# Kernel optimization log

Hardware: AMD Instinct MI355X
Metric: run time of the kernel (lower is better)

The kernel has to match this reference:

```python
import jax, jax.numpy as jnp
import numpy as np

NEG_FILL = -1000000.0


def setup_inputs() -> dict:
    key = jax.random.key(0)
    k1, k2, k3, k4, k5 = jax.random.split(key, 5)
    bs, sl, hd, dd = 128, 512, 1024, 512
    x = jax.random.normal(k1, (bs, sl, hd), dtype=jnp.float32)
    mask = jax.random.randint(k2, (bs, sl), 0, 2) > 0  # bool, True = masked out
    Wq = jax.random.normal(k3, (dd, hd), dtype=jnp.float32)
    bq = jax.random.normal(k4, (dd,), dtype=jnp.float32)
    vq = jax.random.normal(k5, (dd,), dtype=jnp.float32)
    return {"x": x, "mask": mask, "Wq": Wq, "bq": bq, "vq": vq}


def reference(x, mask, Wq, bq, vq):
    # key = tanh(Uq(x)): [bs, sl, dd]
    k = jnp.tanh(jnp.einsum("bsh,dh->bsd", x, Wq) + bq)
    # score = vq . key: [bs, sl]
    score = jnp.einsum("bsd,d->bs", k, vq)
    score = jnp.where(mask, NEG_FILL, score)
    weight = jax.nn.softmax(score, axis=-1)  # [bs, sl]
    # weighted sum over sequence: [bs, hd]
    res = jnp.einsum("bs,bsh->bh", weight, x)
    return res
```

## Files before the change

### kernel.cpp

```cpp
#include <hip/hip_runtime.h>
#include <stdint.h>

#define BS 128
#define SL 512
#define HD 1024
#define DD 512
#define M_TOT (BS*SL)

typedef __attribute__((ext_vector_type(8))) short short8;
typedef __attribute__((ext_vector_type(4))) float f32x4;

__device__ __forceinline__ unsigned short f32_bf16(float f) {
    union { float f; unsigned u; } v; v.f = f;
    unsigned u = v.u + 0x7FFFu + ((v.u >> 16) & 1u);
    return (unsigned short)(u >> 16);
}
__device__ __forceinline__ float bf16_f32(unsigned short h) {
    union { unsigned u; float f; } v; v.u = ((unsigned)h) << 16; return v.f;
}

__global__ void detect_mask_kernel(const unsigned* mw, int* flag) {
    int t = threadIdx.x;
    unsigned bad = 0;
    for (int i = t; i < 1024; i += 256) bad |= (mw[i] > 1u) ? 1u : 0u;
    if (bad) atomicExch(flag, 1);
}

__global__ void pack_wq_kernel(const float* __restrict__ Wq,
                               unsigned short* __restrict__ P) {
    int t = blockIdx.x * 256 + threadIdx.x;
    int d  = t >> 7;
    int h0 = (t & 127) << 3;
    const float* src = Wq + (size_t)d * HD + h0;
    unsigned short hi[8], lo[8];
#pragma unroll
    for (int j = 0; j < 8; ++j) {
        float f = src[j];
        hi[j] = f32_bf16(f);
        lo[j] = f32_bf16(f - bf16_f32(hi[j]));
    }
    int nb = d >> 7, cg = (d >> 4) & 7, lr = d & 15;
    int ks = h0 >> 5, q = (h0 >> 3) & 3;
    int l = q * 16 + lr;
    size_t base = (size_t)(nb * 32 + ks) * 8192 + (size_t)(cg * 64 + l) * 8;
    union { unsigned short s[8]; uint4 v; } a, b;
#pragma unroll
    for (int j = 0; j < 8; ++j) { a.s[j] = hi[j]; b.s[j] = lo[j]; }
    *(uint4*)(P + base)        = a.v;
    *(uint4*)(P + base + 4096) = b.v;
}

__launch_bounds__(256, 2)
__global__ void score_kernel(const float* __restrict__ x,
                             const unsigned short* __restrict__ packW,
                             const float* __restrict__ bq,
                             const float* __restrict__ vq,
                             float* __restrict__ score) {
    __shared__ unsigned short A_hi[4096];
    __shared__ unsigned short A_lo[4096];
    __shared__ unsigned short Bt[8192];

    const int nb = blockIdx.x;
    const int m0 = blockIdx.y * 128;
    const int t = threadIdx.x;
    const int l = t & 63;
    const int w = t >> 6;
    const int wm = w & 1, wn = w >> 1;

    f32x4 acc[4][4];
#pragma unroll
    for (int i = 0; i < 4; ++i)
#pragma unroll
        for (int j = 0; j < 4; ++j)
            acc[i][j] = (f32x4){0.f, 0.f, 0.f, 0.f};

    const uint4* bsrc_base = (const uint4*)packW;

    for (int ks = 0; ks < 32; ++ks) {
        __syncthreads();
#pragma unroll
        for (int r = 0; r < 4; ++r) {
            int idx = r * 256 + t;
            int row = idx >> 3, c4 = idx & 7;
            const float4* xp = (const float4*)(x + (size_t)(m0 + row) * HD + ks * 32);
            float4 v = xp[c4];
            unsigned short h[4], lo4[4];
            float ff[4] = {v.x, v.y, v.z, v.w};
#pragma unroll
            for (int j = 0; j < 4; ++j) {
                h[j]  = f32_bf16(ff[j]);
                lo4[j] = f32_bf16(ff[j] - bf16_f32(h[j]));
            }
            int rg = row >> 4, rr = row & 15, q = c4 >> 1, j0 = (c4 & 1) * 4;
            int off = (rg * 64 + q * 16 + rr) * 8 + j0;
            *(uint2*)&A_hi[off] = make_uint2((unsigned)h[0] | ((unsigned)h[1] << 16),
                                             (unsigned)h[2] | ((unsigned)h[3] << 16));
            *(uint2*)&A_lo[off] = make_uint2((unsigned)lo4[0] | ((unsigned)lo4[1] << 16),
                                             (unsigned)lo4[2] | ((unsigned)lo4[3] << 16));
        }
        {
            const uint4* src = bsrc_base + (size_t)(nb * 32 + ks) * 1024;
            uint4* dst = (uint4*)Bt;
#pragma unroll
            for (int r = 0; r < 4; ++r) dst[r * 256 + t] = src[r * 256 + t];
        }
        __syncthreads();

        const short8* Ah = (const short8*)A_hi;
        const short8* Al = (const short8*)A_lo;
        const short8* Bh = (const short8*)Bt;
        const short8* Bl = (const short8*)(Bt + 4096);
        short8 ah[4], al[4], bh[4], bl[4];
#pragma unroll
        for (int i = 0; i < 4; ++i) {
            ah[i] = Ah[(wm * 4 + i) * 64 + l];
            al[i] = Al[(wm * 4 + i) * 64 + l];
        }
#pragma unroll
        for (int j = 0; j < 4; ++j) {
            bh[j] = Bh[(wn * 4 + j) * 64 + l];
            bl[j] = Bl[(wn * 4 + j) * 64 + l];
        }
#pragma unroll
        for (int i = 0; i < 4; ++i)
#pragma unroll
            for (int j = 0; j < 4; ++j) {
                acc[i][j] = __builtin_amdgcn_mfma_f32_16x16x32_bf16(ah[i], bh[j], acc[i][j], 0, 0, 0);
                acc[i][j] = __builtin_amdgcn_mfma_f32_16x16x32_bf16(al[i], bh[j], acc[i][j], 0, 0, 0);
                acc[i][j] = __builtin_amdgcn_mfma_f32_16x16x32_bf16(ah[i], bl[j], acc[i][j], 0, 0, 0);
            }
    }

    int q = l >> 4, c = l & 15;
#pragma unroll
    for (int i = 0; i < 4; ++i) {
        float rs[4] = {0.f, 0.f, 0.f, 0.f};
#pragma unroll
        for (int j = 0; j < 4; ++j) {
            int n = nb * 128 + wn * 64 + j * 16 + c;
            float bqv = bq[n], vqv = vq[n];
            f32x4 a4 = acc[i][j];
#pragma unroll
            for (int r = 0; r < 4; ++r)
                rs[r] += tanhf(a4[r] + bqv) * vqv;
        }
#pragma unroll
        for (int r = 0; r < 4; ++r) {
            float v = rs[r];
            v += __shfl_xor(v, 1);
            v += __shfl_xor(v, 2);
            v += __shfl_xor(v, 4);
            v += __shfl_xor(v, 8);
            if (c == 0)
                atomicAdd(&score[m0 + wm * 64 + i * 16 + q * 4 + r], v);
        }
    }
}

__global__ void softmax_kernel(const float* __restrict__ score,
                               const void* __restrict__ maskp,
                               const int* __restrict__ flag,
                               float* __restrict__ wgt) {
    __shared__ float red[8];
    int b = blockIdx.x, t = threadIdx.x;
    int w = t >> 6, l = t & 63;
    bool u8 = (*flag != 0);
    int i0 = b * SL + t, i1 = i0 + 256;
    bool mk0, mk1;
    if (u8) {
        mk0 = ((const unsigned char*)maskp)[i0] != 0;
        mk1 = ((const unsigned char*)maskp)[i1] != 0;
    } else {
        mk0 = ((const int*)maskp)[i0] != 0;
        mk1 = ((const int*)maskp)[i1] != 0;
    }
    float s0 = mk0 ? -1000000.0f : score[i0];
    float s1 = mk1 ? -1000000.0f : score[i1];
    float mx = fmaxf(s0, s1);
    for (int d = 1; d < 64; d <<= 1) mx = fmaxf(mx, __shfl_xor(mx, d));
    if (l == 0) red[w] = mx;
    __syncthreads();
    mx = fmaxf(fmaxf(red[0], red[1]), fmaxf(red[2], red[3]));
    float e0 = expf(s0 - mx), e1 = expf(s1 - mx);
    float sm = e0 + e1;
    for (int d = 1; d < 64; d <<= 1) sm += __shfl_xor(sm, d);
    if (l == 0) red[4 + w] = sm;
    __syncthreads();
    sm = red[4] + red[5] + red[6] + red[7];
    float inv = 1.0f / sm;
    wgt[i0] = e0 * inv;
    wgt[i1] = e1 * inv;
}

__global__ void wsum_kernel(const float* __restrict__ x,
                            const float* __restrict__ wgt,
                            float* __restrict__ out) {
    __shared__ float wsh[64];
    int b = blockIdx.x, sc = blockIdx.y, t = threadIdx.x;
    if (t < 64) wsh[t] = wgt[b * SL + sc * 64 + t];
    __syncthreads();
    const float4* xp = (const float4*)(x + ((size_t)b * SL + sc * 64) * HD) + t;
    float ax = 0.f, ay = 0.f, az = 0.f, aw = 0.f;
#pragma unroll 4
    for (int s = 0; s < 64; ++s) {
        float wv = wsh[s];
        float4 v = xp[(size_t)s * 256];
        ax += wv * v.x; ay += wv * v.y; az += wv * v.z; aw += wv * v.w;
    }
    float* dst = out + (size_t)b * HD + t * 4;
    atomicAdd(dst + 0, ax);
    atomicAdd(dst + 1, ay);
    atomicAdd(dst + 2, az);
    atomicAdd(dst + 3, aw);
}

extern "C" void kernel_launch(void* const* d_in, const int* in_sizes, int n_in,
                              void* d_out, int out_size, void* d_ws, size_t ws_size,
                              hipStream_t stream) {
    const float* x  = (const float*)d_in[0];
    const void* mask = d_in[1];
    const float* Wq = (const float*)d_in[2];
    const float* bq = (const float*)d_in[3];
    const float* vq = (const float*)d_in[4];
    float* out = (float*)d_out;

    char* ws = (char*)d_ws;
    unsigned short* packW = (unsigned short*)ws;
    float* score = (float*)(ws + (2u << 20));
    float* wgt   = (float*)(ws + (2u << 20) + (256u << 10));
    int*   flag  = (int*)  (ws + (2u << 20) + (512u << 10));

    hipMemsetAsync(score, 0, M_TOT * sizeof(float), stream);
    hipMemsetAsync(flag, 0, sizeof(int), stream);
    hipMemsetAsync(d_out, 0, (size_t)out_size * sizeof(float), stream);

    detect_mask_kernel<<<1, 256, 0, stream>>>((const unsigned*)mask, flag);
    pack_wq_kernel<<<256, 256, 0, stream>>>(Wq, packW);
    score_kernel<<<dim3(4, 512), 256, 0, stream>>>(x, packW, bq, vq, score);
    softmax_kernel<<<BS, 256, 0, stream>>>(score, mask, flag, wgt);
    wsum_kernel<<<dim3(BS, 8), 256, 0, stream>>>(x, wgt, out);
}
```

Before: 582.2 us.

## Async B-tile loads, swizzled LDS, XCD-aware grid, fast tanh, atomic-free weighted sum

The score GEMM now copies the packed Wq tile into LDS with global_load_lds, which avoids a round trip through registers. The x conversion writes 16-byte chunks into an XOR-swizzled LDS layout to reduce bank conflicts. The grid is flattened and remapped so that blocks sharing an m-tile land on the same XCD for L2 reuse, and launch bounds are raised to 5 waves. tanhf is replaced by an exp-based fast tanh. Mask detection is folded into the pack kernel, memsets are merged, and the weighted-sum atomics are replaced by a partial-write pass plus a reduce kernel. The fast tanh trades a little accuracy for speed, and the higher occupancy target may force register spills.

```diff
diff --git a/kernel.cpp b/kernel.cpp
--- a/kernel.cpp
+++ b/kernel.cpp
@@ -18,39 +18,45 @@
 __device__ __forceinline__ float bf16_f32(unsigned short h) {
     union { unsigned u; float f; } v; v.u = ((unsigned)h) << 16; return v.f;
 }
-
-__global__ void detect_mask_kernel(const unsigned* mw, int* flag) {
-    int t = threadIdx.x;
-    unsigned bad = 0;
-    for (int i = t; i < 1024; i += 256) bad |= (mw[i] > 1u) ? 1u : 0u;
-    if (bad) atomicExch(flag, 1);
+__device__ __forceinline__ float fast_tanh(float x) {
+    float e = __expf(2.0f * x);
+    return 1.0f - 2.0f / (e + 1.0f);
+}
+__device__ __forceinline__ void async_lds16(const void* g, void* l) {
+    __builtin_amdgcn_global_load_lds(
+        (const __attribute__((address_space(1))) unsigned int*)g,
+        (__attribute__((address_space(3))) unsigned int*)l, 16, 0, 0);
 }
 
 __global__ void pack_wq_kernel(const float* __restrict__ Wq,
-                               unsigned short* __restrict__ P) {
+                               unsigned short* __restrict__ P,
+                               const unsigned* __restrict__ mw,
+                               int* __restrict__ flag) {
+    if (blockIdx.x == 0) {
+        unsigned bad = 0;
+        for (int i = threadIdx.x; i < 1024; i += 256) bad |= (mw[i] > 1u) ? 1u : 0u;
+        if (bad) atomicExch(flag, 1);
+    }
     int t = blockIdx.x * 256 + threadIdx.x;
     int d  = t >> 7;
     int h0 = (t & 127) << 3;
     const float* src = Wq + (size_t)d * HD + h0;
-    unsigned short hi[8], lo[8];
+    union { unsigned short s[8]; uint4 v; } a, b;
 #pragma unroll
     for (int j = 0; j < 8; ++j) {
         float f = src[j];
-        hi[j] = f32_bf16(f);
-        lo[j] = f32_bf16(f - bf16_f32(hi[j]));
+        a.s[j] = f32_bf16(f);
+        b.s[j] = f32_bf16(f - bf16_f32(a.s[j]));
     }
     int nb = d >> 7, cg = (d >> 4) & 7, lr = d & 15;
     int ks = h0 >> 5, q = (h0 >> 3) & 3;
     int l = q * 16 + lr;
     size_t base = (size_t)(nb * 32 + ks) * 8192 + (size_t)(cg * 64 + l) * 8;
-    union { unsigned short s[8]; uint4 v; } a, b;
-#pragma unroll
-    for (int j = 0; j < 8; ++j) { a.s[j] = hi[j]; b.s[j] = lo[j]; }
     *(uint4*)(P + base)        = a.v;
     *(uint4*)(P + base + 4096) = b.v;
 }
 
-__launch_bounds__(256, 2)
+__launch_bounds__(256, 5)
 __global__ void score_kernel(const float* __restrict__ x,
                              const unsigned short* __restrict__ packW,
                              const float* __restrict__ bq,
@@ -60,8 +66,12 @@
     __shared__ unsigned short A_lo[4096];
     __shared__ unsigned short Bt[8192];
 
-    const int nb = blockIdx.x;
-    const int m0 = blockIdx.y * 128;
+    const int bid = blockIdx.x;
+    const int xcd = bid & 7;
+    const int slot = bid >> 3;
+    const int nb = slot & 3;
+    const int m0 = (xcd + ((slot >> 2) << 3)) << 7;
+
     const int t = threadIdx.x;
     const int l = t & 63;
     const int w = t >> 6;
@@ -74,47 +84,47 @@
         for (int j = 0; j < 4; ++j)
             acc[i][j] = (f32x4){0.f, 0.f, 0.f, 0.f};
 
-    const uint4* bsrc_base = (const uint4*)packW;
+    const char* Ahc = (const char*)A_hi;
+    const char* Alc = (const char*)A_lo;
 
     for (int ks = 0; ks < 32; ++ks) {
         __syncthreads();
-#pragma unroll
-        for (int r = 0; r < 4; ++r) {
-            int idx = r * 256 + t;
-            int row = idx >> 3, c4 = idx & 7;
-            const float4* xp = (const float4*)(x + (size_t)(m0 + row) * HD + ks * 32);
-            float4 v = xp[c4];
-            unsigned short h[4], lo4[4];
-            float ff[4] = {v.x, v.y, v.z, v.w};
-#pragma unroll
-            for (int j = 0; j < 4; ++j) {
-                h[j]  = f32_bf16(ff[j]);
-                lo4[j] = f32_bf16(ff[j] - bf16_f32(h[j]));
+        {
+            const unsigned short* src = packW + (size_t)(nb * 32 + ks) * 8192;
+            unsigned short* dst = Bt;
+#pragma unroll
+            for (int r = 0; r < 4; ++r)
+                async_lds16(src + (size_t)(r * 256 + t) * 8, dst + (r * 256 + t) * 8);
+        }
+#pragma unroll
+        for (int r = 0; r < 2; ++r) {
+            int u = r * 256 + t;
+            int row = u >> 2, c8 = u & 3;
+            const float4* xp = (const float4*)(x + (size_t)(m0 + row) * HD + ks * 32 + c8 * 8);
+            float4 v0 = xp[0], v1 = xp[1];
+            float ff[8] = {v0.x, v0.y, v0.z, v0.w, v1.x, v1.y, v1.z, v1.w};
+            union { unsigned short s[8]; uint4 q4; } hi, lo;
+#pragma unroll
+            for (int j = 0; j < 8; ++j) {
+                hi.s[j] = f32_bf16(ff[j]);
+                lo.s[j] = f32_bf16(ff[j] - bf16_f32(hi.s[j]));
             }
-            int rg = row >> 4, rr = row & 15, q = c4 >> 1, j0 = (c4 & 1) * 4;
-            int off = (rg * 64 + q * 16 + rr) * 8 + j0;
-            *(uint2*)&A_hi[off] = make_uint2((unsigned)h[0] | ((unsigned)h[1] << 16),
-                                             (unsigned)h[2] | ((unsigned)h[3] << 16));
-            *(uint2*)&A_lo[off] = make_uint2((unsigned)lo4[0] | ((unsigned)lo4[1] << 16),
-                                             (unsigned)lo4[2] | ((unsigned)lo4[3] << 16));
-        }
-        {
-            const uint4* src = bsrc_base + (size_t)(nb * 32 + ks) * 1024;
-            uint4* dst = (uint4*)Bt;
-#pragma unroll
-            for (int r = 0; r < 4; ++r) dst[r * 256 + t] = src[r * 256 + t];
+            int rg = row >> 4, rr = row & 15;
+            int off = (((rg * 64 + c8 * 16 + rr) * 16) ^ (c8 << 5));
+            *(uint4*)((char*)A_hi + off) = hi.q4;
+            *(uint4*)((char*)A_lo + off) = lo.q4;
         }
         __syncthreads();
 
-        const short8* Ah = (const short8*)A_hi;
-        const short8* Al = (const short8*)A_lo;
         const short8* Bh = (const short8*)Bt;
         const short8* Bl = (const short8*)(Bt + 4096);
         short8 ah[4], al[4], bh[4], bl[4];
+        const int xr = (l >> 4) << 5;
 #pragma unroll
         for (int i = 0; i < 4; ++i) {
-            ah[i] = Ah[(wm * 4 + i) * 64 + l];
-            al[i] = Al[(wm * 4 + i) * 64 + l];
+            int off = ((((wm * 4 + i) * 64 + l) * 16) ^ xr);
+            ah[i] = *(const short8*)(Ahc + off);
+            al[i] = *(const short8*)(Alc + off);
         }
 #pragma unroll
         for (int j = 0; j < 4; ++j) {
@@ -142,7 +152,7 @@
             f32x4 a4 = acc[i][j];
 #pragma unroll
             for (int r = 0; r < 4; ++r)
-                rs[r] += tanhf(a4[r] + bqv) * vqv;
+                rs[r] += fast_tanh(a4[r] + bqv) * vqv;
         }
 #pragma unroll
         for (int r = 0; r < 4; ++r) {
@@ -192,9 +202,9 @@
     wgt[i1] = e1 * inv;
 }
 
-__global__ void wsum_kernel(const float* __restrict__ x,
-                            const float* __restrict__ wgt,
-                            float* __restrict__ out) {
+__global__ void wsum_partial_kernel(const float* __restrict__ x,
+                                    const float* __restrict__ wgt,
+                                    float* __restrict__ partial) {
     __shared__ float wsh[64];
     int b = blockIdx.x, sc = blockIdx.y, t = threadIdx.x;
     if (t < 64) wsh[t] = wgt[b * SL + sc * 64 + t];
@@ -207,11 +217,22 @@
         float4 v = xp[(size_t)s * 256];
         ax += wv * v.x; ay += wv * v.y; az += wv * v.z; aw += wv * v.w;
     }
-    float* dst = out + (size_t)b * HD + t * 4;
-    atomicAdd(dst + 0, ax);
-    atomicAdd(dst + 1, ay);
-    atomicAdd(dst + 2, az);
-    atomicAdd(dst + 3, aw);
+    float4 r = {ax, ay, az, aw};
+    ((float4*)(partial + (size_t)(b * 8 + sc) * HD))[t] = r;
+}
+
+__global__ void wsum_reduce_kernel(const float* __restrict__ partial,
+                                   float* __restrict__ out) {
+    int i = blockIdx.x * 256 + threadIdx.x;
+    int b = i >> 8, h4 = i & 255;
+    const float4* p = (const float4*)partial + (size_t)b * 8 * 256 + h4;
+    float4 a = p[0];
+#pragma unroll
+    for (int sc = 1; sc < 8; ++sc) {
+        float4 v = p[sc * 256];
+        a.x += v.x; a.y += v.y; a.z += v.z; a.w += v.w;
+    }
+    ((float4*)out)[i] = a;
 }
 
 extern "C" void kernel_launch(void* const* d_in, const int* in_sizes, int n_in,
@@ -226,17 +247,16 @@
 
     char* ws = (char*)d_ws;
     unsigned short* packW = (unsigned short*)ws;
-    float* score = (float*)(ws + (2u << 20));
-    float* wgt   = (float*)(ws + (2u << 20) + (256u << 10));
-    int*   flag  = (int*)  (ws + (2u << 20) + (512u << 10));
-
-    hipMemsetAsync(score, 0, M_TOT * sizeof(float), stream);
-    hipMemsetAsync(flag, 0, sizeof(int), stream);
-    hipMemsetAsync(d_out, 0, (size_t)out_size * sizeof(float), stream);
-
-    detect_mask_kernel<<<1, 256, 0, stream>>>((const unsigned*)mask, flag);
-    pack_wq_kernel<<<256, 256, 0, stream>>>(Wq, packW);
-    score_kernel<<<dim3(4, 512), 256, 0, stream>>>(x, packW, bq, vq, score);
+    float* score   = (float*)(ws + (2u << 20));
+    int*   flag    = (int*)  (ws + (2u << 20) + (256u << 10));
+    float* wgt     = (float*)(ws + (2u << 20) + (257u << 10));
+    float* partial = (float*)(ws + (3u << 20));
+
+    hipMemsetAsync(score, 0, (256u << 10) + 4, stream);
+
+    pack_wq_kernel<<<256, 256, 0, stream>>>(Wq, packW, (const unsigned*)mask, flag);
+    score_kernel<<<2048, 256, 0, stream>>>(x, packW, bq, vq, score);
     softmax_kernel<<<BS, 256, 0, stream>>>(score, mask, flag, wgt);
-    wsum_kernel<<<dim3(BS, 8), 256, 0, stream>>>(x, wgt, out);
-}
+    wsum_partial_kernel<<<dim3(BS, 8), 256, 0, stream>>>(x, wgt, partial);
+    wsum_reduce_kernel<<<128, 256, 0, stream>>>(partial, out);
+}
```

Result: slower. 1.057 ms (+81.5%).

## Drop LDS staging in score GEMM, fuse softmax with weighted sum, remove atomics

Applied to the files above, without the earlier changes.

The score GEMM now loads x and the packed Wq straight from global memory into registers in MFMA fragment layout. This removes the LDS staging and both barriers per k-step, and occupancy is raised to 3 blocks. The hi/lo split is done by truncation with byte permutes, tanh uses an exp-based approximation, and the block order is remapped per XCD for L2 locality. Score partials go to 8 separate slices instead of atomics, and mask detection, softmax and the weighted sum are fused into one kernel without memsets or atomics. Global loads no longer share reuse through LDS, and the truncated hi split and fast tanh slightly change the numerics.

```diff
diff --git a/kernel.cpp b/kernel.cpp
--- a/kernel.cpp
+++ b/kernel.cpp
@@ -10,20 +10,9 @@
 typedef __attribute__((ext_vector_type(8))) short short8;
 typedef __attribute__((ext_vector_type(4))) float f32x4;
 
-__device__ __forceinline__ unsigned short f32_bf16(float f) {
-    union { float f; unsigned u; } v; v.f = f;
-    unsigned u = v.u + 0x7FFFu + ((v.u >> 16) & 1u);
-    return (unsigned short)(u >> 16);
-}
-__device__ __forceinline__ float bf16_f32(unsigned short h) {
-    union { unsigned u; float f; } v; v.u = ((unsigned)h) << 16; return v.f;
-}
-
-__global__ void detect_mask_kernel(const unsigned* mw, int* flag) {
-    int t = threadIdx.x;
-    unsigned bad = 0;
-    for (int i = t; i < 1024; i += 256) bad |= (mw[i] > 1u) ? 1u : 0u;
-    if (bad) atomicExch(flag, 1);
+__device__ __forceinline__ float fast_tanh(float x) {
+    float e = __expf(2.0f * x);
+    return 1.0f - 2.0f / (e + 1.0f);
 }
 
 __global__ void pack_wq_kernel(const float* __restrict__ Wq,
@@ -32,41 +21,45 @@
     int d  = t >> 7;
     int h0 = (t & 127) << 3;
     const float* src = Wq + (size_t)d * HD + h0;
-    unsigned short hi[8], lo[8];
+    union { unsigned short s[8]; uint4 v; } a, b;
 #pragma unroll
     for (int j = 0; j < 8; ++j) {
-        float f = src[j];
-        hi[j] = f32_bf16(f);
-        lo[j] = f32_bf16(f - bf16_f32(hi[j]));
+        union { float f; unsigned u; } v; v.f = src[j];
+        unsigned hi = v.u & 0xFFFF0000u;
+        float lo = v.f - __uint_as_float(hi);
+        unsigned lu = __float_as_uint(lo);
+        lu = lu + 0x7FFFu + ((lu >> 16) & 1u);
+        a.s[j] = (unsigned short)(hi >> 16);
+        b.s[j] = (unsigned short)(lu >> 16);
     }
     int nb = d >> 7, cg = (d >> 4) & 7, lr = d & 15;
     int ks = h0 >> 5, q = (h0 >> 3) & 3;
     int l = q * 16 + lr;
     size_t base = (size_t)(nb * 32 + ks) * 8192 + (size_t)(cg * 64 + l) * 8;
-    union { unsigned short s[8]; uint4 v; } a, b;
-#pragma unroll
-    for (int j = 0; j < 8; ++j) { a.s[j] = hi[j]; b.s[j] = lo[j]; }
     *(uint4*)(P + base)        = a.v;
     *(uint4*)(P + base + 4096) = b.v;
 }
 
-__launch_bounds__(256, 2)
+__launch_bounds__(256, 3)
 __global__ void score_kernel(const float* __restrict__ x,
                              const unsigned short* __restrict__ packW,
                              const float* __restrict__ bq,
                              const float* __restrict__ vq,
-                             float* __restrict__ score) {
-    __shared__ unsigned short A_hi[4096];
-    __shared__ unsigned short A_lo[4096];
-    __shared__ unsigned short Bt[8192];
-
-    const int nb = blockIdx.x;
-    const int m0 = blockIdx.y * 128;
+                             float* __restrict__ scorep) {
+    const int bid = blockIdx.x;
+    const int xcd = bid & 7;
+    const int slot = bid >> 3;
+    const int nb = slot & 3;
+    const int m0 = (xcd + ((slot >> 2) << 3)) << 7;
+
     const int t = threadIdx.x;
     const int l = t & 63;
     const int w = t >> 6;
     const int wm = w & 1, wn = w >> 1;
 
+    const int lr = l & 15;
+    const int lk = l >> 4;
+
     f32x4 acc[4][4];
 #pragma unroll
     for (int i = 0; i < 4; ++i)
@@ -74,64 +67,48 @@
         for (int j = 0; j < 4; ++j)
             acc[i][j] = (f32x4){0.f, 0.f, 0.f, 0.f};
 
-    const uint4* bsrc_base = (const uint4*)packW;
+    const float* xb = x + (size_t)(m0 + wm * 64 + lr) * HD + lk * 8;
+    const unsigned short* wb = packW + (size_t)nb * 32 * 8192 + (wn * 4) * 512 + l * 8;
 
     for (int ks = 0; ks < 32; ++ks) {
-        __syncthreads();
-#pragma unroll
-        for (int r = 0; r < 4; ++r) {
-            int idx = r * 256 + t;
-            int row = idx >> 3, c4 = idx & 7;
-            const float4* xp = (const float4*)(x + (size_t)(m0 + row) * HD + ks * 32);
-            float4 v = xp[c4];
-            unsigned short h[4], lo4[4];
-            float ff[4] = {v.x, v.y, v.z, v.w};
+        short8 bh[4], bl[4];
+        const unsigned short* wp = wb + ks * 8192;
+#pragma unroll
+        for (int j = 0; j < 4; ++j) {
+            bh[j] = *(const short8*)(wp + j * 512);
+            bl[j] = *(const short8*)(wp + j * 512 + 4096);
+        }
+        const float* xk = xb + ks * 32;
+#pragma unroll
+        for (int i = 0; i < 4; ++i) {
+            float4 v0 = *(const float4*)(xk + (size_t)i * 16 * HD);
+            float4 v1 = *(const float4*)(xk + (size_t)i * 16 * HD + 4);
+            unsigned a[8] = {
+                __float_as_uint(v0.x), __float_as_uint(v0.y),
+                __float_as_uint(v0.z), __float_as_uint(v0.w),
+                __float_as_uint(v1.x), __float_as_uint(v1.y),
+                __float_as_uint(v1.z), __float_as_uint(v1.w)};
+            union { unsigned u[4]; short8 v; } H, L;
+#pragma unroll
+            for (int p = 0; p < 4; ++p) {
+                unsigned e0 = a[2 * p], e1 = a[2 * p + 1];
+                float l0 = __uint_as_float(e0) - __uint_as_float(e0 & 0xFFFF0000u);
+                float l1 = __uint_as_float(e1) - __uint_as_float(e1 & 0xFFFF0000u);
+                H.u[p] = __builtin_amdgcn_perm(e1, e0, 0x07060302u);
+                L.u[p] = __builtin_amdgcn_perm(__float_as_uint(l1),
+                                               __float_as_uint(l0), 0x07060302u);
+            }
 #pragma unroll
             for (int j = 0; j < 4; ++j) {
-                h[j]  = f32_bf16(ff[j]);
-                lo4[j] = f32_bf16(ff[j] - bf16_f32(h[j]));
+                acc[i][j] = __builtin_amdgcn_mfma_f32_16x16x32_bf16(H.v, bh[j], acc[i][j], 0, 0, 0);
+                acc[i][j] = __builtin_amdgcn_mfma_f32_16x16x32_bf16(L.v, bh[j], acc[i][j], 0, 0, 0);
+                acc[i][j] = __builtin_amdgcn_mfma_f32_16x16x32_bf16(H.v, bl[j], acc[i][j], 0, 0, 0);
             }
-            int rg = row >> 4, rr = row & 15, q = c4 >> 1, j0 = (c4 & 1) * 4;
-            int off = (rg * 64 + q * 16 + rr) * 8 + j0;
-            *(uint2*)&A_hi[off] = make_uint2((unsigned)h[0] | ((unsigned)h[1] << 16),
-                                             (unsigned)h[2] | ((unsigned)h[3] << 16));
-            *(uint2*)&A_lo[off] = make_uint2((unsigned)lo4[0] | ((unsigned)lo4[1] << 16),
-                                             (unsigned)lo4[2] | ((unsigned)lo4[3] << 16));
-        }
-        {
-            const uint4* src = bsrc_base + (size_t)(nb * 32 + ks) * 1024;
-            uint4* dst = (uint4*)Bt;
-#pragma unroll
-            for (int r = 0; r < 4; ++r) dst[r * 256 + t] = src[r * 256 + t];
-        }
-        __syncthreads();
-
-        const short8* Ah = (const short8*)A_hi;
-        const short8* Al = (const short8*)A_lo;
-        const short8* Bh = (const short8*)Bt;
-        const short8* Bl = (const short8*)(Bt + 4096);
-        short8 ah[4], al[4], bh[4], bl[4];
-#pragma unroll
-        for (int i = 0; i < 4; ++i) {
-            ah[i] = Ah[(wm * 4 + i) * 64 + l];
-            al[i] = Al[(wm * 4 + i) * 64 + l];
-        }
-#pragma unroll
-        for (int j = 0; j < 4; ++j) {
-            bh[j] = Bh[(wn * 4 + j) * 64 + l];
-            bl[j] = Bl[(wn * 4 + j) * 64 + l];
-        }
-#pragma unroll
-        for (int i = 0; i < 4; ++i)
-#pragma unroll
-            for (int j = 0; j < 4; ++j) {
-                acc[i][j] = __builtin_amdgcn_mfma_f32_16x16x32_bf16(ah[i], bh[j], acc[i][j], 0, 0, 0);
-                acc[i][j] = __builtin_amdgcn_mfma_f32_16x16x32_bf16(al[i], bh[j], acc[i][j], 0, 0, 0);
-                acc[i][j] = __builtin_amdgcn_mfma_f32_16x16x32_bf16(ah[i], bl[j], acc[i][j], 0, 0, 0);
-            }
+        }
     }
 
     int q = l >> 4, c = l & 15;
+    float* myslice = scorep + (size_t)(nb * 2 + wn) * M_TOT;
 #pragma unroll
     for (int i = 0; i < 4; ++i) {
         float rs[4] = {0.f, 0.f, 0.f, 0.f};
@@ -142,7 +119,7 @@
             f32x4 a4 = acc[i][j];
 #pragma unroll
             for (int r = 0; r < 4; ++r)
-                rs[r] += tanhf(a4[r] + bqv) * vqv;
+                rs[r] += fast_tanh(a4[r] + bqv) * vqv;
         }
 #pragma unroll
         for (int r = 0; r < 4; ++r) {
@@ -152,66 +129,80 @@
             v += __shfl_xor(v, 4);
             v += __shfl_xor(v, 8);
             if (c == 0)
-                atomicAdd(&score[m0 + wm * 64 + i * 16 + q * 4 + r], v);
-        }
-    }
-}
-
-__global__ void softmax_kernel(const float* __restrict__ score,
-                               const void* __restrict__ maskp,
-                               const int* __restrict__ flag,
-                               float* __restrict__ wgt) {
+                myslice[m0 + wm * 64 + i * 16 + q * 4 + r] = v;
+        }
+    }
+}
+
+__global__ void out_kernel(const float* __restrict__ x,
+                           const float* __restrict__ scorep,
+                           const void* __restrict__ maskp,
+                           float* __restrict__ out) {
+    __shared__ float wsh[SL];
+    __shared__ float psh[4 * 256];
     __shared__ float red[8];
-    int b = blockIdx.x, t = threadIdx.x;
-    int w = t >> 6, l = t & 63;
-    bool u8 = (*flag != 0);
-    int i0 = b * SL + t, i1 = i0 + 256;
+    __shared__ int flags[4];
+
+    const int b = blockIdx.x, hs = blockIdx.y, t = threadIdx.x;
+    const int w = t >> 6, l = t & 63;
+
+    const unsigned* mw = (const unsigned*)maskp;
+    int bad = (mw[t] > 1u) || (mw[t + 256] > 1u) ||
+              (mw[t + 512] > 1u) || (mw[t + 768] > 1u);
+    bad = __any(bad);
+    if (l == 0) flags[w] = bad;
+    __syncthreads();
+    const bool u8 = (flags[0] | flags[1] | flags[2] | flags[3]) != 0;
+
+    int s0 = t, s1 = t + 256;
+    float sc0 = 0.f, sc1 = 0.f;
+#pragma unroll
+    for (int p = 0; p < 8; ++p) {
+        sc0 += scorep[(size_t)p * M_TOT + b * SL + s0];
+        sc1 += scorep[(size_t)p * M_TOT + b * SL + s1];
+    }
     bool mk0, mk1;
     if (u8) {
-        mk0 = ((const unsigned char*)maskp)[i0] != 0;
-        mk1 = ((const unsigned char*)maskp)[i1] != 0;
+        mk0 = ((const unsigned char*)maskp)[b * SL + s0] != 0;
+        mk1 = ((const unsigned char*)maskp)[b * SL + s1] != 0;
     } else {
-        mk0 = ((const int*)maskp)[i0] != 0;
-        mk1 = ((const int*)maskp)[i1] != 0;
-    }
-    float s0 = mk0 ? -1000000.0f : score[i0];
-    float s1 = mk1 ? -1000000.0f : score[i1];
-    float mx = fmaxf(s0, s1);
+        mk0 = ((const int*)maskp)[b * SL + s0] != 0;
+        mk1 = ((const int*)maskp)[b * SL + s1] != 0;
+    }
+    float v0 = mk0 ? -1000000.0f : sc0;
+    float v1 = mk1 ? -1000000.0f : sc1;
+    float mx = fmaxf(v0, v1);
     for (int d = 1; d < 64; d <<= 1) mx = fmaxf(mx, __shfl_xor(mx, d));
     if (l == 0) red[w] = mx;
     __syncthreads();
     mx = fmaxf(fmaxf(red[0], red[1]), fmaxf(red[2], red[3]));
-    float e0 = expf(s0 - mx), e1 = expf(s1 - mx);
+    float e0 = expf(v0 - mx), e1 = expf(v1 - mx);
     float sm = e0 + e1;
     for (int d = 1; d < 64; d <<= 1) sm += __shfl_xor(sm, d);
     if (l == 0) red[4 + w] = sm;
     __syncthreads();
     sm = red[4] + red[5] + red[6] + red[7];
     float inv = 1.0f / sm;
-    wgt[i0] = e0 * inv;
-    wgt[i1] = e1 * inv;
-}
-
-__global__ void wsum_kernel(const float* __restrict__ x,
-                            const float* __restrict__ wgt,
-                            float* __restrict__ out) {
-    __shared__ float wsh[64];
-    int b = blockIdx.x, sc = blockIdx.y, t = threadIdx.x;
-    if (t < 64) wsh[t] = wgt[b * SL + sc * 64 + t];
-    __syncthreads();
-    const float4* xp = (const float4*)(x + ((size_t)b * SL + sc * 64) * HD) + t;
+    wsh[s0] = e0 * inv;
+    wsh[s1] = e1 * inv;
+    __syncthreads();
+
+    const float* xp = x + ((size_t)b * SL + w * 128) * HD + hs * 256 + l * 4;
     float ax = 0.f, ay = 0.f, az = 0.f, aw = 0.f;
-#pragma unroll 4
-    for (int s = 0; s < 64; ++s) {
-        float wv = wsh[s];
-        float4 v = xp[(size_t)s * 256];
+#pragma unroll 8
+    for (int s = 0; s < 128; ++s) {
+        float wv = wsh[w * 128 + s];
+        float4 v = *(const float4*)(xp + (size_t)s * HD);
         ax += wv * v.x; ay += wv * v.y; az += wv * v.z; aw += wv * v.w;
     }
-    float* dst = out + (size_t)b * HD + t * 4;
-    atomicAdd(dst + 0, ax);
-    atomicAdd(dst + 1, ay);
-    atomicAdd(dst + 2, az);
-    atomicAdd(dst + 3, aw);
+    psh[w * 256 + l * 4 + 0] = ax;
+    psh[w * 256 + l * 4 + 1] = ay;
+    psh[w * 256 + l * 4 + 2] = az;
+    psh[w * 256 + l * 4 + 3] = aw;
+    __syncthreads();
+
+    float r0 = psh[t] + psh[256 + t] + psh[512 + t] + psh[768 + t];
+    out[(size_t)b * HD + hs * 256 + t] = r0;
 }
 
 extern "C" void kernel_launch(void* const* d_in, const int* in_sizes, int n_in,
@@ -226,17 +217,9 @@
 
     char* ws = (char*)d_ws;
     unsigned short* packW = (unsigned short*)ws;
-    float* score = (float*)(ws + (2u << 20));
-    float* wgt   = (float*)(ws + (2u << 20) + (256u << 10));
-    int*   flag  = (int*)  (ws + (2u << 20) + (512u << 10));
-
-    hipMemsetAsync(score, 0, M_TOT * sizeof(float), stream);
-    hipMemsetAsync(flag, 0, sizeof(int), stream);
-    hipMemsetAsync(d_out, 0, (size_t)out_size * sizeof(float), stream);
-
-    detect_mask_kernel<<<1, 256, 0, stream>>>((const unsigned*)mask, flag);
+    float* scorep = (float*)(ws + (2u << 20));
+
     pack_wq_kernel<<<256, 256, 0, stream>>>(Wq, packW);
-    score_kernel<<<dim3(4, 512), 256, 0, stream>>>(x, packW, bq, vq, score);
-    softmax_kernel<<<BS, 256, 0, stream>>>(score, mask, flag, wgt);
-    wsum_kernel<<<dim3(BS, 8), 256, 0, stream>>>(x, wgt, out);
-}
+    score_kernel<<<2048, 256, 0, stream>>>(x, packW, bq, vq, scorep);
+    out_kernel<<<dim3(BS, 4), 256, 0, stream>>>(x, scorep, mask, out);
+}
```

Result: slower. 658.9 us (+13.2%).
